# Performance work log

Hardware: AMD Instinct MI355X
Metric: run time of the kernel (lower is better)

## Reference

```python
import jax, jax.numpy as jnp
import numpy as np

# Lorentz (hyperboloid) manifold, curvature parameter K: x0 = sqrt(K + ||x_space||^2)
K = 1.0
LN_EPS = 1e-5
PROJ_EPS = 1e-6
L, D, H, B, S, V = 12, 512, 8, 2, 1024, 50257
DH = D // H  # 64 space dims per head


def add_time(space):
    # lift space components onto the hyperboloid
    t = jnp.sqrt(jnp.sum(space * space, axis=-1, keepdims=True) + K)
    return jnp.concatenate([t, space], axis=-1)


def l_project(z):
    # renormalize an ambient vector onto the hyperboloid (Lorentz midpoint / LResNet normalization)
    inner = -jnp.square(z[..., :1]) + jnp.sum(jnp.square(z[..., 1:]), axis=-1, keepdims=True)
    return jnp.sqrt(K) * z / jnp.sqrt(jnp.clip(-inner, PROJ_EPS, None))


def l_layernorm(x, g, b):
    # LayerNorm on the space part, recompute time
    s = x[..., 1:]
    mu = jnp.mean(s, axis=-1, keepdims=True)
    var = jnp.var(s, axis=-1, keepdims=True)
    s = (s - mu) * jax.lax.rsqrt(var + LN_EPS) * g + b
    return add_time(s)


def setup_inputs() -> dict:
    key = jax.random.key(0)
    ks = jax.random.split(key, 12)
    std_in = D ** -0.5
    std_out = (2 * D * L) ** -0.5  # out_proj_std from the torch init
    inp = {}
    inp['text_tokens'] = jax.random.randint(ks[0], (B, S), 0, V)
    inp['embed_table'] = jax.random.normal(ks[1], (V, D - 1), jnp.float32) * 0.02
    inp['Wq'] = jax.random.normal(ks[2], (L, D, D), jnp.float32) * std_in
    inp['bq'] = jnp.zeros((L, D), jnp.float32)
    inp['Wk'] = jax.random.normal(ks[3], (L, D, D), jnp.float32) * std_in
    inp['bk'] = jnp.zeros((L, D), jnp.float32)
    inp['Wv'] = jax.random.normal(ks[4], (L, D, D), jnp.float32) * std_in
    inp['bv'] = jnp.zeros((L, D), jnp.float32)
    inp['Wo'] = jax.random.normal(ks[5], (L, H * (DH + 1), D - 1), jnp.float32) * std_in
    inp['bo'] = jnp.zeros((L, D - 1), jnp.float32)
    inp['ln1_g'] = jnp.ones((L, D - 1), jnp.float32)
    inp['ln1_b'] = jnp.zeros((L, D - 1), jnp.float32)
    inp['ln2_g'] = jnp.ones((L, D - 1), jnp.float32)
    inp['ln2_b'] = jnp.zeros((L, D - 1), jnp.float32)
    inp['Wfc'] = jax.random.normal(ks[6], (L, D, 4 * D - 1), jnp.float32) * std_in
    inp['bfc'] = jnp.zeros((L, 4 * D - 1), jnp.float32)
    inp['Wpr'] = jax.random.normal(ks[7], (L, 4 * D, D - 1), jnp.float32) * std_out
    inp['bpr'] = jnp.zeros((L, D - 1), jnp.float32)
    inp['res_w1'] = jnp.ones((L,), jnp.float32)
    inp['res_w2'] = jnp.ones((L,), jnp.float32)
    inp['Wfin'] = jax.random.normal(ks[8], (D, D - 1), jnp.float32) * std_in
    inp['bfin'] = jnp.zeros((D - 1,), jnp.float32)
    inp['lnf_g'] = jnp.ones((D - 1,), jnp.float32)
    inp['lnf_b'] = jnp.zeros((D - 1,), jnp.float32)
    return inp


def reference(text_tokens, embed_table, Wq, bq, Wk, bk, Wv, bv, Wo, bo, ln1_g, ln1_b,
              ln2_g, ln2_b, Wfc, bfc, Wpr, bpr, res_w1, res_w2, Wfin, bfin, lnf_g, lnf_b):
    b, s = text_tokens.shape
    scale = 1.0 / np.sqrt(DH)
    # LorentzEmbeddings: space-part lookup, time recomputed
    x = add_time(embed_table[text_tokens])  # [B, S, D]
    causal = jnp.tril(jnp.ones((s, s), bool))  # True = attend
    for i in range(L):
        # --- Lorentz multi-head self-attention ---
        lx = l_layernorm(x, ln1_g[i], ln1_b[i])
        q = add_time((lx @ Wq[i] + bq[i]).reshape(b, s, H, DH))  # [B,S,H,DH+1]
        k = add_time((lx @ Wk[i] + bk[i]).reshape(b, s, H, DH))
        v = add_time((lx @ Wv[i] + bv[i]).reshape(b, s, H, DH))
        qm = jnp.concatenate([-q[..., :1], q[..., 1:]], axis=-1)  # apply Minkowski metric
        linner = jnp.einsum('bihd,bjhd->bhij', qm, k)  # Lorentz inner product <q_i, k_j>_L
        scores = (2.0 * K + 2.0 * linner) * scale     # = -d_L^2(q,k)/sqrt(dh)
        scores = jnp.where(causal[None, None], scores, -1e9)
        a = jax.nn.softmax(scores, axis=-1)
        agg = jnp.einsum('bhij,bjhd->bihd', a, v)      # Lorentz centroid numerator
        agg = l_project(agg)                           # normalize back to hyperboloid
        ax = add_time(agg.reshape(b, s, H * (DH + 1)) @ Wo[i] + bo[i])  # heads-concat proj
        x = l_project(x + res_w1[i] * ax)              # LResNet residual 1
        # --- Lorentz MLP ---
        h = l_layernorm(x, ln2_g[i], ln2_b[i])
        h = add_time(h @ Wfc[i] + bfc[i])              # c_fc: D -> 4D ambient
        h = add_time(jax.nn.gelu(h[..., 1:]))          # LorentzActivation (GELU on space)
        h = add_time(h @ Wpr[i] + bpr[i])              # c_proj: 4D -> D ambient
        x = l_project(x + res_w2[i] * h)               # LResNet residual 2
    x = add_time(x @ Wfin + bfin)                      # final_proj
    x = l_layernorm(x, lnf_g, lnf_b)                   # ln_final
    return x
```

## Files before the change

kernel.cpp:

```cpp
#include <hip/hip_runtime.h>
#include <cstdint>

#define DEV __device__ __forceinline__

typedef _Float16 f16;
typedef _Float16 f16x8 __attribute__((ext_vector_type(8)));
typedef float f32x4 __attribute__((ext_vector_type(4)));
typedef unsigned int u32;

DEV void gll16(const void* g, void* l) {
  __builtin_amdgcn_global_load_lds((const __attribute__((address_space(1))) u32*)g,
                                   (__attribute__((address_space(3))) u32*)l, 16, 0, 0);
}

DEV float block_sum(float v, float* red) {
#pragma unroll
  for (int o = 32; o; o >>= 1) v += __shfl_xor(v, o);
  int w = threadIdx.x >> 6;
  __syncthreads();
  if ((threadIdx.x & 63) == 0) red[w] = v;
  __syncthreads();
  return red[0] + red[1] + red[2] + red[3];
}

__global__ void k_trans(const float* __restrict__ W0, f16* __restrict__ BT0, int K, int N, int Kpad,
                        size_t srcStride, size_t dstStride) {
  __shared__ float t[32][33];
  const float* W = W0 + (size_t)blockIdx.z * srcStride;
  f16* BT = BT0 + (size_t)blockIdx.z * dstStride;
  int n0 = blockIdx.x * 32, k0 = blockIdx.y * 32, tx = threadIdx.x, ty = threadIdx.y;
  for (int i = ty; i < 32; i += 8) {
    int k = k0 + i, n = n0 + tx;
    t[i][tx] = (k < K && n < N) ? W[(size_t)k * N + n] : 0.f;
  }
  __syncthreads();
  for (int i = ty; i < 32; i += 8)
    BT[(size_t)(n0 + i) * Kpad + k0 + tx] = (f16)t[tx][i];
}

__global__ void k_trans3(const float* __restrict__ Wq, const float* __restrict__ Wk,
                         const float* __restrict__ Wv, f16* __restrict__ BT) {
  __shared__ float t[32][33];
  const int layer = blockIdx.z / 3, typ = blockIdx.z % 3;
  const float* W = ((typ == 0) ? Wq : (typ == 1) ? Wk : Wv) + (size_t)layer * 262144;
  f16* dst = BT + (size_t)layer * 786432 + (size_t)typ * 262144;
  int n0 = blockIdx.x * 32, k0 = blockIdx.y * 32, tx = threadIdx.x, ty = threadIdx.y;
  for (int i = ty; i < 32; i += 8) t[i][tx] = W[(size_t)(k0 + i) * 512 + n0 + tx];
  __syncthreads();
  for (int i = ty; i < 32; i += 8) dst[(size_t)(n0 + i) * 512 + k0 + tx] = (f16)t[tx][i];
}

template <int BM, int BN, int EPI>
__launch_bounds__(256)
__global__ void k_gemm(const f16* __restrict__ A, const f16* __restrict__ BT,
                       int lda, int ldb, int klen,
                       float* __restrict__ O1, float* __restrict__ O2, int ldc,
                       const float* __restrict__ c0, const float* __restrict__ c1,
                       const float* __restrict__ c2, float* __restrict__ ssq,
                       f16* __restrict__ H1, f16* __restrict__ H2, f16* __restrict__ H3) {
  constexpr int FM = BM / 32, FN = BN / 32;
  __shared__ f16 sA[BM * 64];
  __shared__ f16 sB[BN * 64];
  const int tid = threadIdx.x, wid = tid >> 6, lane = tid & 63;
  const int l15 = lane & 15, l4 = lane >> 4;
  const int m0 = blockIdx.x * BM, n0 = blockIdx.y * BN;
  const int wm = wid >> 1, wn = wid & 1;
  const int kbeg = blockIdx.z * klen;
  f32x4 acc[FM][FN];
#pragma unroll
  for (int i = 0; i < FM; i++)
#pragma unroll
    for (int j = 0; j < FN; j++) acc[i][j] = (f32x4){0.f, 0.f, 0.f, 0.f};
  const size_t ldab = (size_t)lda * 2, ldbb = (size_t)ldb * 2;
  const int swz = ((lane & 7) ^ (lane >> 3)) * 16;
  const char* Ab = (const char*)A + (size_t)m0 * ldab + (size_t)(lane >> 3) * ldab + swz;
  const char* Bb = (const char*)BT + (size_t)n0 * ldbb + (size_t)(lane >> 3) * ldbb + swz;
  for (int k0 = kbeg; k0 < kbeg + klen; k0 += 64) {
    for (int i = wid; i < BM / 8; i += 4)
      gll16(Ab + (size_t)(i * 8) * ldab + (size_t)k0 * 2, (char*)sA + i * 1024);
    for (int i = wid; i < BN / 8; i += 4)
      gll16(Bb + (size_t)(i * 8) * ldbb + (size_t)k0 * 2, (char*)sB + i * 1024);
    __syncthreads();
#pragma unroll
    for (int kk = 0; kk < 2; kk++) {
      f16x8 af[FM], bf[FN];
#pragma unroll
      for (int i = 0; i < FM; i++) {
        int row = wm * (BM / 2) + i * 16 + l15;
        af[i] = *(const f16x8*)(sA + row * 64 + (((kk * 4 + l4) ^ (l15 & 7)) * 8));
      }
#pragma unroll
      for (int j = 0; j < FN; j++) {
        int row = wn * (BN / 2) + j * 16 + l15;
        bf[j] = *(const f16x8*)(sB + row * 64 + (((kk * 4 + l4) ^ (l15 & 7)) * 8));
      }
#pragma unroll
      for (int i = 0; i < FM; i++)
#pragma unroll
        for (int j = 0; j < FN; j++)
          acc[i][j] = __builtin_amdgcn_mfma_f32_16x16x32_f16(af[i], bf[j], acc[i][j], 0, 0, 0);
    }
    __syncthreads();
  }
  if (EPI == 0) {
#pragma unroll
    for (int i = 0; i < FM; i++) {
      int row0 = m0 + wm * (BM / 2) + i * 16 + l4 * 4;
#pragma unroll
      for (int j = 0; j < FN; j++) {
        int col = n0 + wn * (BN / 2) + j * 16 + l15;
#pragma unroll
        for (int r = 0; r < 4; r++) O1[(size_t)(row0 + r) * ldc + col] = acc[i][j][r];
      }
    }
  } else if (EPI == 1) {
    const int cb = (n0 >> 6) + wn;
    const int typ = cb >> 3, h = cb & 7;
    const float* bb = (typ == 0) ? c0 : (typ == 1) ? c1 : c2;
    float bias_j[FN];
#pragma unroll
    for (int j = 0; j < FN; j++) bias_j[j] = bb[h * 64 + j * 16 + l15];
    const float qs = (typ == 0) ? 0.25f : 1.0f;
#pragma unroll
    for (int i = 0; i < FM; i++) {
#pragma unroll
      for (int r = 0; r < 4; r++) {
        float y[FN];
        float ss = 0.f;
#pragma unroll
        for (int j = 0; j < FN; j++) {
          y[j] = acc[i][j][r] + bias_j[j];
          ss += y[j] * y[j];
        }
        ss += __shfl_xor(ss, 1); ss += __shfl_xor(ss, 2);
        ss += __shfl_xor(ss, 4); ss += __shfl_xor(ss, 8);
        float t = sqrtf(ss + 1.f);
        int row = m0 + wm * 64 + i * 16 + l4 * 4 + r;
        int b = row >> 10, s = row & 1023, bh = b * 8 + h;
        if (typ < 2) {
          f16* dst = (typ == 0) ? H1 : H2;
          size_t base = ((size_t)bh * 1024 + s) * 88;
#pragma unroll
          for (int j = 0; j < FN; j++) dst[base + j * 16 + l15] = (f16)(qs * y[j]);
          if (l15 == 0) dst[base + 64] = (f16)(qs * t);
        } else {
#pragma unroll
          for (int j = 0; j < FN; j++)
            H3[((size_t)bh * 80 + j * 16 + l15) * 1024 + s] = (f16)y[j];
          if (l15 == 0) H3[((size_t)bh * 80 + 64) * 1024 + s] = (f16)t;
        }
      }
    }
  } else if (EPI == 2) {
#pragma unroll
    for (int i = 0; i < FM; i++) {
#pragma unroll
      for (int r = 0; r < 4; r++) {
        int row = m0 + wm * 64 + i * 16 + l4 * 4 + r;
        float ss = 0.f;
#pragma unroll
        for (int j = 0; j < FN; j++) {
          int col = n0 + wn * 64 + j * 16 + l15;
          float gg = 0.f;
          if (col < 2047) {
            float yv = acc[i][j][r] + c0[col];
            float cc = yv * yv * yv;
            gg = 0.5f * yv * (1.f + tanhf(0.7978845608f * (yv + 0.044715f * cc)));
          }
          ss += gg * gg;
          H1[(size_t)row * 2048 + col] = (f16)gg;
        }
        ss += __shfl_xor(ss, 1); ss += __shfl_xor(ss, 2);
        ss += __shfl_xor(ss, 4); ss += __shfl_xor(ss, 8);
        if (l15 == 0) atomicAdd(ssq + row, ss);
      }
    }
  } else {
    float* O = blockIdx.z ? O2 : O1;
#pragma unroll
    for (int i = 0; i < FM; i++) {
#pragma unroll
      for (int r = 0; r < 4; r++) {
        int row = m0 + wm * (BM / 2) + i * 16 + l4 * 4 + r;
        float t = 0.f;
        if (blockIdx.z == 0) t = sqrtf(ssq[row] + 1.f);
#pragma unroll
        for (int j = 0; j < FN; j++) {
          int col = n0 + wn * (BN / 2) + j * 16 + l15;
          float v = acc[i][j][r];
          if (blockIdx.z == 0) v += t * ((col < 511) ? c0[col] : 0.f);
          O[(size_t)row * ldc + col] = v;
        }
      }
    }
  }
}

__global__ void k_embed(const int* __restrict__ tok, const float* __restrict__ tbl,
                        const float* __restrict__ g, const float* __restrict__ bsh,
                        float* __restrict__ x, f16* __restrict__ act) {
  __shared__ float red[4];
  const int m = blockIdx.x, tid = threadIdx.x;
  const float* e = tbl + (size_t)tok[m] * 511;
  float e0 = (tid < 511) ? e[tid] : 0.f;
  float e1 = (tid + 256 < 511) ? e[tid + 256] : 0.f;
  float s1 = block_sum(e0 + e1, red);
  float s2 = block_sum(e0 * e0 + e1 * e1, red);
  float t = sqrtf(s2 + 1.f);
  float* xr = x + (size_t)m * 512;
  if (tid == 0) xr[0] = t;
  if (tid < 511) xr[1 + tid] = e0;
  if (tid + 256 < 511) xr[257 + tid] = e1;
  float mu = s1 / 511.f;
  float var = s2 / 511.f - mu * mu;
  float inv = rsqrtf(var + 1e-5f);
  float n0 = (tid < 511) ? (e0 - mu) * inv * g[tid] + bsh[tid] : 0.f;
  float n1 = (tid + 256 < 511) ? (e1 - mu) * inv * g[tid + 256] + bsh[tid + 256] : 0.f;
  float sn = block_sum(n0 * n0 + n1 * n1, red);
  float t2 = sqrtf(sn + 1.f);
  f16* ar = act + (size_t)m * 512;
  if (tid == 0) ar[0] = (f16)t2;
  if (tid < 511) ar[1 + tid] = (f16)n0;
  if (tid + 256 < 511) ar[257 + tid] = (f16)n1;
}

__launch_bounds__(64)
__global__ void k_attn(const f16* __restrict__ qhat, const f16* __restrict__ khat,
                       const f16* __restrict__ vT, f16* __restrict__ ao) {
  __shared__ f16 sP[16 * 88];
  const int bid = blockIdx.x, bh = bid & 15, rt = 63 - (bid >> 4);
  const int lane = threadIdx.x, l15 = lane & 15, l4 = lane >> 4;
  const f16* qp = qhat + ((size_t)bh * 1024 + rt * 16) * 88;
  const f16* kp = khat + (size_t)bh * 1024 * 88;
  const f16* vp = vT + (size_t)bh * 80 * 1024;
  f16x8 qf0 = *(const f16x8*)(qp + l15 * 88 + l4 * 8);
  f16x8 qf1 = *(const f16x8*)(qp + l15 * 88 + 32 + l4 * 8);
  float qth[4];
#pragma unroll
  for (int r = 0; r < 4; r++) qth[r] = (float)qp[(l4 * 4 + r) * 88 + 64];
  f32x4 acc[5];
#pragma unroll
  for (int i = 0; i < 5; i++) acc[i] = (f32x4){0, 0, 0, 0};
  float mrun[4] = {-3e38f, -3e38f, -3e38f, -3e38f}, lrun[4] = {0, 0, 0, 0};
  const int nt = (rt >> 2) + 1;
  for (int jt = 0; jt < nt; ++jt) {
    const int j0 = jt * 64;
    const bool dt = (jt == nt - 1);
    f32x4 sc[4];
#pragma unroll
    for (int fn = 0; fn < 4; fn++) {
      const f16* kb = kp + (size_t)(j0 + fn * 16 + l15) * 88;
      f16x8 k0v = *(const f16x8*)(kb + l4 * 8);
      f16x8 k1v = *(const f16x8*)(kb + 32 + l4 * 8);
      f32x4 a = (f32x4){0, 0, 0, 0};
      a = __builtin_amdgcn_mfma_f32_16x16x32_f16(qf0, k0v, a, 0, 0, 0);
      a = __builtin_amdgcn_mfma_f32_16x16x32_f16(qf1, k1v, a, 0, 0, 0);
      sc[fn] = a;
    }
    float s[4][4];
#pragma unroll
    for (int fn = 0; fn < 4; fn++) {
      float ktc = (float)kp[(size_t)(j0 + fn * 16 + l15) * 88 + 64];
      int col = j0 + fn * 16 + l15;
#pragma unroll
      for (int r = 0; r < 4; r++) {
        int row = rt * 16 + l4 * 4 + r;
        float v = sc[fn][r] - qth[r] * ktc;
        s[fn][r] = (!dt || col <= row) ? v : -3e38f;
      }
    }
    float mnew[4], al[4], rs[4];
#pragma unroll
    for (int r = 0; r < 4; r++) {
      float t = fmaxf(fmaxf(s[0][r], s[1][r]), fmaxf(s[2][r], s[3][r]));
#pragma unroll
      for (int o = 8; o; o >>= 1) t = fmaxf(t, __shfl_xor(t, o));
      mnew[r] = fmaxf(mrun[r], t);
      al[r] = exp2f((mrun[r] - mnew[r]) * 1.44269504f);
      mrun[r] = mnew[r];
      rs[r] = 0.f;
    }
#pragma unroll
    for (int fn = 0; fn < 4; fn++)
#pragma unroll
      for (int r = 0; r < 4; r++) {
        float p = exp2f((s[fn][r] - mnew[r]) * 1.44269504f);
        rs[r] += p;
        sP[(l4 * 4 + r) * 88 + fn * 16 + l15] = (f16)p;
      }
#pragma unroll
    for (int r = 0; r < 4; r++) {
#pragma unroll
      for (int o = 8; o; o >>= 1) rs[r] += __shfl_xor(rs[r], o);
      lrun[r] = lrun[r] * al[r] + rs[r];
    }
#pragma unroll
    for (int fd = 0; fd < 5; fd++)
#pragma unroll
      for (int r = 0; r < 4; r++) acc[fd][r] *= al[r];
    __syncthreads();
#pragma unroll
    for (int ks = 0; ks < 2; ks++) {
      f16x8 pf = *(const f16x8*)(sP + l15 * 88 + ks * 32 + l4 * 8);
#pragma unroll
      for (int fd = 0; fd < 5; fd++) {
        f16x8 vf = *(const f16x8*)(vp + (size_t)(fd * 16 + l15) * 1024 + j0 + ks * 32 + l4 * 8);
        acc[fd] = __builtin_amdgcn_mfma_f32_16x16x32_f16(pf, vf, acc[fd], 0, 0, 0);
      }
    }
    __syncthreads();
  }
  const int b = bh >> 3, h = bh & 7;
#pragma unroll
  for (int r = 0; r < 4; r++) {
    float invl = 1.0f / lrun[r];
    float ss = 0.f;
    float ov[4];
#pragma unroll
    for (int fd = 0; fd < 4; fd++) {
      ov[fd] = acc[fd][r] * invl;
      ss += ov[fd] * ov[fd];
    }
#pragma unroll
    for (int o = 8; o; o >>= 1) ss += __shfl_xor(ss, o);
    float tv = acc[4][r] * invl;
    tv = __shfl(tv, lane & 48);
    float scp = rsqrtf(fmaxf(tv * tv - ss, 1e-6f));
    int row = rt * 16 + l4 * 4 + r;
    size_t rowbase = ((size_t)b * 1024 + row) * 576;
    size_t rb = rowbase + h * 65;
    if (l15 == 0) ao[rb] = (f16)(tv * scp);
#pragma unroll
    for (int fd = 0; fd < 4; fd++) ao[rb + 1 + fd * 16 + l15] = (f16)(ov[fd] * scp);
    for (int c = l15; c < 56; c += 16) ao[rowbase + 520 + c] = (f16)0.f;
  }
}

__global__ void k_resproj(float* __restrict__ x, const float* __restrict__ r1,
                          const float* __restrict__ r2, int useR2,
                          const float* __restrict__ bias, const float* __restrict__ resw, int li,
                          const float* __restrict__ g, const float* __restrict__ bsh,
                          f16* __restrict__ act, int applyLN, float* __restrict__ ssq) {
  __shared__ float red[4];
  const int m = blockIdx.x, tid = threadIdx.x;
  const float* ra = r1 + (size_t)m * 512;
  const float* rb = r2 + (size_t)m * 512;
  float* xr = x + (size_t)m * 512;
  const float rw = resw[li];
  if (tid == 0) ssq[m] = 0.f;
  float y0 = 0.f, y1 = 0.f;
  if (tid < 511) { y0 = ra[tid] + bias[tid]; if (useR2) y0 += rb[tid]; }
  if (tid + 256 < 511) { y1 = ra[tid + 256] + bias[tid + 256]; if (useR2) y1 += rb[tid + 256]; }
  float s2 = block_sum(y0 * y0 + y1 * y1, red);
  float tax = sqrtf(s2 + 1.f);
  float xt = xr[0];
  float u0 = (tid < 511) ? xr[1 + tid] + rw * y0 : 0.f;
  float u1 = (tid + 256 < 511) ? xr[257 + tid] + rw * y1 : 0.f;
  float ut = xt + rw * tax;
  float su = block_sum(u0 + u1, red);
  float su2 = block_sum(u0 * u0 + u1 * u1, red);
  float scp = rsqrtf(fmaxf(ut * ut - su2, 1e-6f));
  float nx0 = u0 * scp, nx1 = u1 * scp, nxt = ut * scp;
  if (tid == 0) xr[0] = nxt;
  if (tid < 511) xr[1 + tid] = nx0;
  if (tid + 256 < 511) xr[257 + tid] = nx1;
  f16* ar = act + (size_t)m * 512;
  if (applyLN) {
    float mu = su * scp / 511.f;
    float var = su2 * scp * scp / 511.f - mu * mu;
    float inv = rsqrtf(var + 1e-5f);
    float n0 = (tid < 511) ? (nx0 - mu) * inv * g[tid] + bsh[tid] : 0.f;
    float n1 = (tid + 256 < 511) ? (nx1 - mu) * inv * g[tid + 256] + bsh[tid + 256] : 0.f;
    float sn = block_sum(n0 * n0 + n1 * n1, red);
    float t2 = sqrtf(sn + 1.f);
    if (tid == 0) ar[0] = (f16)t2;
    if (tid < 511) ar[1 + tid] = (f16)n0;
    if (tid + 256 < 511) ar[257 + tid] = (f16)n1;
  } else {
    if (tid == 0) ar[0] = (f16)nxt;
    if (tid < 511) ar[1 + tid] = (f16)nx0;
    if (tid + 256 < 511) ar[257 + tid] = (f16)nx1;
  }
}

__global__ void k_final(const float* __restrict__ raw, const float* __restrict__ bias,
                        const float* __restrict__ g, const float* __restrict__ bsh,
                        float* __restrict__ out) {
  __shared__ float red[4];
  const int m = blockIdx.x, tid = threadIdx.x;
  const float* rr = raw + (size_t)m * 512;
  float y0 = (tid < 511) ? rr[tid] + bias[tid] : 0.f;
  float y1 = (tid + 256 < 511) ? rr[tid + 256] + bias[tid + 256] : 0.f;
  float s1 = block_sum(y0 + y1, red);
  float s2 = block_sum(y0 * y0 + y1 * y1, red);
  float mu = s1 / 511.f;
  float var = s2 / 511.f - mu * mu;
  float inv = rsqrtf(var + 1e-5f);
  float n0 = (tid < 511) ? (y0 - mu) * inv * g[tid] + bsh[tid] : 0.f;
  float n1 = (tid + 256 < 511) ? (y1 - mu) * inv * g[tid + 256] + bsh[tid + 256] : 0.f;
  float sn = block_sum(n0 * n0 + n1 * n1, red);
  float t2 = sqrtf(sn + 1.f);
  float* orow = out + (size_t)m * 512;
  if (tid == 0) orow[0] = t2;
  if (tid < 511) orow[1 + tid] = n0;
  if (tid + 256 < 511) orow[257 + tid] = n1;
}

extern "C" void kernel_launch(void* const* d_in, const int* in_sizes, int n_in,
                              void* d_out, int out_size, void* d_ws, size_t ws_size,
                              hipStream_t stream) {
  (void)in_sizes; (void)n_in; (void)out_size; (void)ws_size;
  const int* tok = (const int*)d_in[0];
  const float* etab = (const float*)d_in[1];
  const float* Wq = (const float*)d_in[2];
  const float* bq = (const float*)d_in[3];
  const float* Wk = (const float*)d_in[4];
  const float* bk = (const float*)d_in[5];
  const float* Wv = (const float*)d_in[6];
  const float* bv = (const float*)d_in[7];
  const float* Wo = (const float*)d_in[8];
  const float* bo = (const float*)d_in[9];
  const float* ln1g = (const float*)d_in[10];
  const float* ln1b = (const float*)d_in[11];
  const float* ln2g = (const float*)d_in[12];
  const float* ln2b = (const float*)d_in[13];
  const float* Wfc = (const float*)d_in[14];
  const float* bfc = (const float*)d_in[15];
  const float* Wpr = (const float*)d_in[16];
  const float* bpr = (const float*)d_in[17];
  const float* rw1 = (const float*)d_in[18];
  const float* rw2 = (const float*)d_in[19];
  const float* Wfin = (const float*)d_in[20];
  const float* bfin = (const float*)d_in[21];
  const float* lnfg = (const float*)d_in[22];
  const float* lnfb = (const float*)d_in[23];

  char* wsb = (char*)d_ws;
  size_t off = 0;
  auto alloc = [&](size_t bytes) -> char* {
    char* p = wsb + off;
    off = (off + bytes + 1023) & ~(size_t)1023;
    return p;
  };
  float* x = (float*)alloc(2048ull * 512 * 4);
  f16* actA = (f16*)alloc(2048ull * 512 * 2);
  float* raw1 = (float*)alloc(2048ull * 512 * 4);
  float* raw2 = (float*)alloc(2048ull * 512 * 4);
  float* ssq = (float*)alloc(2048ull * 4);
  f16* qhat = (f16*)alloc(16ull * 1024 * 88 * 2);
  f16* khat = (f16*)alloc(16ull * 1024 * 88 * 2);
  f16* vT = (f16*)alloc(16ull * 80 * 1024 * 2);
  f16* ao = (f16*)alloc(2048ull * 576 * 2);
  f16* fcact = (f16*)alloc(2048ull * 2048 * 2);
  f16* wqkvT = (f16*)alloc(12ull * 1536 * 512 * 2);
  f16* woT = (f16*)alloc(12ull * 512 * 576 * 2);
  f16* wfcT = (f16*)alloc(12ull * 2048 * 512 * 2);
  f16* wprT = (f16*)alloc(12ull * 512 * 2048 * 2);
  f16* wfinT = (f16*)alloc(512ull * 512 * 2);

  k_trans3<<<dim3(16, 16, 36), dim3(32, 8), 0, stream>>>(Wq, Wk, Wv, wqkvT);
  k_trans<<<dim3(16, 18, 12), dim3(32, 8), 0, stream>>>(Wo, woT, 520, 511, 576,
                                                        520ull * 511, 512ull * 576);
  k_trans<<<dim3(64, 16, 12), dim3(32, 8), 0, stream>>>(Wfc, wfcT, 512, 2047, 512,
                                                        512ull * 2047, 2048ull * 512);
  k_trans<<<dim3(16, 64, 12), dim3(32, 8), 0, stream>>>(Wpr + 511, wprT, 2047, 511, 2048,
                                                        2048ull * 511, 512ull * 2048);
  k_trans<<<dim3(16, 16, 1), dim3(32, 8), 0, stream>>>(Wfin, wfinT, 512, 511, 512, 0, 0);

  k_embed<<<2048, 256, 0, stream>>>(tok, etab, ln1g, ln1b, x, actA);

  for (int li = 0; li < 12; li++) {
    const f16* wqkvT_l = wqkvT + (size_t)li * 1536 * 512;
    const f16* woT_l = woT + (size_t)li * 512 * 576;
    const f16* wfcT_l = wfcT + (size_t)li * 2048 * 512;
    const f16* wprT_l = wprT + (size_t)li * 512 * 2048;
    const float* Wpr_l = Wpr + (size_t)li * 2048 * 511;
    const float* bq_l = bq + (size_t)li * 512;
    const float* bk_l = bk + (size_t)li * 512;
    const float* bv_l = bv + (size_t)li * 512;
    const float* bo_l = bo + (size_t)li * 511;
    const float* bfc_l = bfc + (size_t)li * 2047;
    const float* bpr_l = bpr + (size_t)li * 511;
    const float* ln2g_l = ln2g + (size_t)li * 511;
    const float* ln2b_l = ln2b + (size_t)li * 511;

    k_gemm<128, 128, 1><<<dim3(16, 12, 1), 256, 0, stream>>>(
        actA, wqkvT_l, 512, 512, 512, nullptr, nullptr, 0,
        bq_l, bk_l, bv_l, nullptr, qhat, khat, vT);
    k_attn<<<1024, 64, 0, stream>>>(qhat, khat, vT, ao);
    k_gemm<64, 64, 0><<<dim3(32, 8, 1), 256, 0, stream>>>(
        ao, woT_l, 576, 576, 576, raw1, nullptr, 512,
        nullptr, nullptr, nullptr, nullptr, nullptr, nullptr, nullptr);
    k_resproj<<<2048, 256, 0, stream>>>(x, raw1, raw1, 0, bo_l, rw1, li,
                                        ln2g_l, ln2b_l, actA, 1, ssq);
    k_gemm<128, 128, 2><<<dim3(16, 16, 1), 256, 0, stream>>>(
        actA, wfcT_l, 512, 512, 512, nullptr, nullptr, 0,
        bfc_l, nullptr, nullptr, ssq, fcact, nullptr, nullptr);
    k_gemm<64, 64, 3><<<dim3(32, 8, 2), 256, 0, stream>>>(
        fcact, wprT_l, 2048, 2048, 1024, raw1, raw2, 512,
        Wpr_l, nullptr, nullptr, ssq, nullptr, nullptr, nullptr);
    const float* ng = (li < 11) ? ln1g + (size_t)(li + 1) * 511 : ln1g;
    const float* nb = (li < 11) ? ln1b + (size_t)(li + 1) * 511 : ln1b;
    k_resproj<<<2048, 256, 0, stream>>>(x, raw1, raw2, 1, bpr_l, rw2, li,
                                        ng, nb, actA, (li < 11) ? 1 : 0, ssq);
  }

  k_gemm<64, 64, 0><<<dim3(32, 8, 1), 256, 0, stream>>>(
      actA, wfinT, 512, 512, 512, raw1, nullptr, 512,
      nullptr, nullptr, nullptr, nullptr, nullptr, nullptr, nullptr);
  k_final<<<2048, 256, 0, stream>>>(raw1, bfin, lnfg, lnfb, (float*)d_out);
}
```

Before: 1.650 ms.

## Double-buffer GEMM LDS loads, remap blocks across XCDs, split-K four for c_proj

The GEMM kernel now stages the next 64-wide K slice into a second LDS buffer while the current one is consumed, synchronising with explicit vmcnt waits and raw barriers instead of a load-then-sync loop. 128-row tiles run with 8 waves per block. Block indices are remapped so neighbouring tiles land on the same XCD, in both the GEMM and the attention kernel. The c_proj GEMM goes from split-K 2 to split-K 4, with four partial buffers summed in the residual kernel. Attention also drops its per-iteration block barriers, which is safe because the block is a single wave. The aim is to hide global-load latency and improve cache locality and occupancy, at the cost of more LDS per block and extra partial-sum traffic.

```diff
diff --git a/kernel.cpp b/kernel.cpp
--- a/kernel.cpp
+++ b/kernel.cpp
@@ -1,12 +1,12 @@
 #include <hip/hip_runtime.h>
 #include <cstdint>
-
-#define DEV __device__ __forceinline__
 
 typedef _Float16 f16;
 typedef _Float16 f16x8 __attribute__((ext_vector_type(8)));
 typedef float f32x4 __attribute__((ext_vector_type(4)));
 typedef unsigned int u32;
+
+#define DEV __device__ __forceinline__
 
 DEV void gll16(const void* g, void* l) {
   __builtin_amdgcn_global_load_lds((const __attribute__((address_space(1))) u32*)g,
@@ -50,65 +50,93 @@
   for (int i = ty; i < 32; i += 8) dst[(size_t)(n0 + i) * 512 + k0 + tx] = (f16)t[tx][i];
 }
 
-template <int BM, int BN, int EPI>
-__launch_bounds__(256)
-__global__ void k_gemm(const f16* __restrict__ A, const f16* __restrict__ BT,
-                       int lda, int ldb, int klen,
-                       float* __restrict__ O1, float* __restrict__ O2, int ldc,
-                       const float* __restrict__ c0, const float* __restrict__ c1,
-                       const float* __restrict__ c2, float* __restrict__ ssq,
-                       f16* __restrict__ H1, f16* __restrict__ H2, f16* __restrict__ H3) {
-  constexpr int FM = BM / 32, FN = BN / 32;
-  __shared__ f16 sA[BM * 64];
-  __shared__ f16 sB[BN * 64];
+template <int BM, int BN, int KZ, int EPI>
+__global__ __launch_bounds__((BM == 128) ? 512 : 256)
+void k_gemm(const f16* __restrict__ A, const f16* __restrict__ B,
+            int lda, int ldb, int klen, int GM,
+            float* __restrict__ O1, float* __restrict__ O2,
+            float* __restrict__ O3, float* __restrict__ O4, int ldc,
+            const float* __restrict__ c0, const float* __restrict__ c1,
+            const float* __restrict__ c2, float* __restrict__ ssq,
+            f16* __restrict__ H1, f16* __restrict__ H2, f16* __restrict__ H3) {
+  constexpr int NW = (BM == 128) ? 8 : 4;
+  constexpr int WM = (BM == 128) ? 4 : 2;
+  constexpr int FN = BN / ((NW / WM) * 16);
   const int tid = threadIdx.x, wid = tid >> 6, lane = tid & 63;
   const int l15 = lane & 15, l4 = lane >> 4;
-  const int m0 = blockIdx.x * BM, n0 = blockIdx.y * BN;
-  const int wm = wid >> 1, wn = wid & 1;
-  const int kbeg = blockIdx.z * klen;
-  f32x4 acc[FM][FN];
-#pragma unroll
-  for (int i = 0; i < FM; i++)
+  const int wm = wid % WM, wn = wid / WM;
+  const int nwg = gridDim.x;
+  int lin = blockIdx.x;
+  int wg = (lin & 7) * (nwg >> 3) + (lin >> 3);
+  int tn = wg / (GM * KZ);
+  int rem = wg - tn * (GM * KZ);
+  int tm = rem / KZ, tz = rem - (rem / KZ) * KZ;
+  const int m0 = tm * BM, n0 = tn * BN, kbeg = tz * klen, ksteps = klen / 64;
+  __shared__ __align__(16) char SM[(BM + BN) * 256];
+  f32x4 acc[2][FN];
+#pragma unroll
+  for (int i = 0; i < 2; i++)
 #pragma unroll
     for (int j = 0; j < FN; j++) acc[i][j] = (f32x4){0.f, 0.f, 0.f, 0.f};
   const size_t ldab = (size_t)lda * 2, ldbb = (size_t)ldb * 2;
   const int swz = ((lane & 7) ^ (lane >> 3)) * 16;
-  const char* Ab = (const char*)A + (size_t)m0 * ldab + (size_t)(lane >> 3) * ldab + swz;
-  const char* Bb = (const char*)BT + (size_t)n0 * ldbb + (size_t)(lane >> 3) * ldbb + swz;
-  for (int k0 = kbeg; k0 < kbeg + klen; k0 += 64) {
-    for (int i = wid; i < BM / 8; i += 4)
-      gll16(Ab + (size_t)(i * 8) * ldab + (size_t)k0 * 2, (char*)sA + i * 1024);
-    for (int i = wid; i < BN / 8; i += 4)
-      gll16(Bb + (size_t)(i * 8) * ldbb + (size_t)k0 * 2, (char*)sB + i * 1024);
-    __syncthreads();
+  const char* Ab = (const char*)A + (size_t)(m0 + (lane >> 3)) * ldab + swz + (size_t)kbeg * 2;
+  const char* Bb = (const char*)B + (size_t)(n0 + (lane >> 3)) * ldbb + swz + (size_t)kbeg * 2;
+  auto stage = [&](int buf, int ks) {
+    char* da = SM + buf * (BM * 128);
+    char* db = SM + 2 * BM * 128 + buf * (BN * 128);
+    for (int i = wid; i < BM / 8; i += NW)
+      gll16(Ab + (size_t)(i * 8) * ldab + (size_t)ks * 128, da + i * 1024);
+    for (int i = wid; i < BN / 8; i += NW)
+      gll16(Bb + (size_t)(i * 8) * ldbb + (size_t)ks * 128, db + i * 1024);
+  };
+  stage(0, 0);
+  asm volatile("s_waitcnt vmcnt(0)" ::: "memory");
+  __builtin_amdgcn_s_barrier();
+  __builtin_amdgcn_sched_barrier(0);
+  int cur = 0;
+  for (int ks = 0; ks < ksteps; ks++) {
+    const bool more = (ks + 1 < ksteps);
+    if (more) {
+      stage(cur ^ 1, ks + 1);
+      asm volatile("s_waitcnt vmcnt(4)" ::: "memory");
+    } else {
+      asm volatile("s_waitcnt vmcnt(0)" ::: "memory");
+    }
+    __builtin_amdgcn_s_barrier();
+    __builtin_amdgcn_sched_barrier(0);
+    const f16* sA = (const f16*)(SM + cur * (BM * 128));
+    const f16* sB = (const f16*)(SM + 2 * BM * 128 + cur * (BN * 128));
 #pragma unroll
     for (int kk = 0; kk < 2; kk++) {
-      f16x8 af[FM], bf[FN];
-#pragma unroll
-      for (int i = 0; i < FM; i++) {
-        int row = wm * (BM / 2) + i * 16 + l15;
+      f16x8 af[2], bf[FN];
+#pragma unroll
+      for (int i = 0; i < 2; i++) {
+        int row = wm * 32 + i * 16 + l15;
         af[i] = *(const f16x8*)(sA + row * 64 + (((kk * 4 + l4) ^ (l15 & 7)) * 8));
       }
 #pragma unroll
       for (int j = 0; j < FN; j++) {
-        int row = wn * (BN / 2) + j * 16 + l15;
+        int row = wn * (FN * 16) + j * 16 + l15;
         bf[j] = *(const f16x8*)(sB + row * 64 + (((kk * 4 + l4) ^ (l15 & 7)) * 8));
       }
 #pragma unroll
-      for (int i = 0; i < FM; i++)
+      for (int i = 0; i < 2; i++)
 #pragma unroll
         for (int j = 0; j < FN; j++)
           acc[i][j] = __builtin_amdgcn_mfma_f32_16x16x32_f16(af[i], bf[j], acc[i][j], 0, 0, 0);
     }
-    __syncthreads();
+    __builtin_amdgcn_sched_barrier(0);
+    __builtin_amdgcn_s_barrier();
+    cur ^= 1;
   }
   if (EPI == 0) {
 #pragma unroll
-    for (int i = 0; i < FM; i++) {
-      int row0 = m0 + wm * (BM / 2) + i * 16 + l4 * 4;
+    for (int i = 0; i < 2; i++) {
+      int row0 = m0 + wm * 32 + i * 16 + l4 * 4;
 #pragma unroll
       for (int j = 0; j < FN; j++) {
-        int col = n0 + wn * (BN / 2) + j * 16 + l15;
+        int col = n0 + wn * (FN * 16) + j * 16 + l15;
 #pragma unroll
         for (int r = 0; r < 4; r++) O1[(size_t)(row0 + r) * ldc + col] = acc[i][j][r];
       }
@@ -117,28 +145,24 @@
     const int cb = (n0 >> 6) + wn;
     const int typ = cb >> 3, h = cb & 7;
     const float* bb = (typ == 0) ? c0 : (typ == 1) ? c1 : c2;
-    float bias_j[FN];
-#pragma unroll
-    for (int j = 0; j < FN; j++) bias_j[j] = bb[h * 64 + j * 16 + l15];
+    float bj[FN];
+#pragma unroll
+    for (int j = 0; j < FN; j++) bj[j] = bb[h * 64 + j * 16 + l15];
     const float qs = (typ == 0) ? 0.25f : 1.0f;
 #pragma unroll
-    for (int i = 0; i < FM; i++) {
+    for (int i = 0; i < 2; i++) {
 #pragma unroll
       for (int r = 0; r < 4; r++) {
-        float y[FN];
-        float ss = 0.f;
-#pragma unroll
-        for (int j = 0; j < FN; j++) {
-          y[j] = acc[i][j][r] + bias_j[j];
-          ss += y[j] * y[j];
-        }
+        float y[FN], ss = 0.f;
+#pragma unroll
+        for (int j = 0; j < FN; j++) { y[j] = acc[i][j][r] + bj[j]; ss += y[j] * y[j]; }
         ss += __shfl_xor(ss, 1); ss += __shfl_xor(ss, 2);
         ss += __shfl_xor(ss, 4); ss += __shfl_xor(ss, 8);
         float t = sqrtf(ss + 1.f);
-        int row = m0 + wm * 64 + i * 16 + l4 * 4 + r;
+        int row = m0 + wm * 32 + i * 16 + l4 * 4 + r;
         int b = row >> 10, s = row & 1023, bh = b * 8 + h;
         if (typ < 2) {
-          f16* dst = (typ == 0) ? H1 : H2;
+          f16* dst = typ ? H2 : H1;
           size_t base = ((size_t)bh * 1024 + s) * 88;
 #pragma unroll
           for (int j = 0; j < FN; j++) dst[base + j * 16 + l15] = (f16)(qs * y[j]);
@@ -153,14 +177,14 @@
     }
   } else if (EPI == 2) {
 #pragma unroll
-    for (int i = 0; i < FM; i++) {
+    for (int i = 0; i < 2; i++) {
 #pragma unroll
       for (int r = 0; r < 4; r++) {
-        int row = m0 + wm * 64 + i * 16 + l4 * 4 + r;
+        int row = m0 + wm * 32 + i * 16 + l4 * 4 + r;
         float ss = 0.f;
 #pragma unroll
         for (int j = 0; j < FN; j++) {
-          int col = n0 + wn * 64 + j * 16 + l15;
+          int col = n0 + wn * (FN * 16) + j * 16 + l15;
           float gg = 0.f;
           if (col < 2047) {
             float yv = acc[i][j][r] + c0[col];
@@ -176,19 +200,19 @@
       }
     }
   } else {
-    float* O = blockIdx.z ? O2 : O1;
-#pragma unroll
-    for (int i = 0; i < FM; i++) {
+    float* O = (tz == 0) ? O1 : (tz == 1) ? O2 : (tz == 2) ? O3 : O4;
+#pragma unroll
+    for (int i = 0; i < 2; i++) {
 #pragma unroll
       for (int r = 0; r < 4; r++) {
-        int row = m0 + wm * (BM / 2) + i * 16 + l4 * 4 + r;
+        int row = m0 + wm * 32 + i * 16 + l4 * 4 + r;
         float t = 0.f;
-        if (blockIdx.z == 0) t = sqrtf(ssq[row] + 1.f);
+        if (tz == 0) t = sqrtf(ssq[row] + 1.f);
 #pragma unroll
         for (int j = 0; j < FN; j++) {
-          int col = n0 + wn * (BN / 2) + j * 16 + l15;
+          int col = n0 + wn * (FN * 16) + j * 16 + l15;
           float v = acc[i][j][r];
-          if (blockIdx.z == 0) v += t * ((col < 511) ? c0[col] : 0.f);
+          if (tz == 0) v += t * ((col < 511) ? c0[col] : 0.f);
           O[(size_t)row * ldc + col] = v;
         }
       }
@@ -228,7 +252,9 @@
 __global__ void k_attn(const f16* __restrict__ qhat, const f16* __restrict__ khat,
                        const f16* __restrict__ vT, f16* __restrict__ ao) {
   __shared__ f16 sP[16 * 88];
-  const int bid = blockIdx.x, bh = bid & 15, rt = 63 - (bid >> 4);
+  const int lin = blockIdx.x;
+  const int wg = (lin & 7) * 128 + (lin >> 3);
+  const int bh = wg >> 6, rt = 63 - (wg & 63);
   const int lane = threadIdx.x, l15 = lane & 15, l4 = lane >> 4;
   const f16* qp = qhat + ((size_t)bh * 1024 + rt * 16) * 88;
   const f16* kp = khat + (size_t)bh * 1024 * 88;
@@ -298,7 +324,8 @@
     for (int fd = 0; fd < 5; fd++)
 #pragma unroll
       for (int r = 0; r < 4; r++) acc[fd][r] *= al[r];
-    __syncthreads();
+    asm volatile("s_waitcnt lgkmcnt(0)" ::: "memory");
+    __builtin_amdgcn_sched_barrier(0);
 #pragma unroll
     for (int ks = 0; ks < 2; ks++) {
       f16x8 pf = *(const f16x8*)(sP + l15 * 88 + ks * 32 + l4 * 8);
@@ -308,19 +335,14 @@
         acc[fd] = __builtin_amdgcn_mfma_f32_16x16x32_f16(pf, vf, acc[fd], 0, 0, 0);
       }
     }
-    __syncthreads();
   }
   const int b = bh >> 3, h = bh & 7;
 #pragma unroll
   for (int r = 0; r < 4; r++) {
     float invl = 1.0f / lrun[r];
-    float ss = 0.f;
-    float ov[4];
-#pragma unroll
-    for (int fd = 0; fd < 4; fd++) {
-      ov[fd] = acc[fd][r] * invl;
-      ss += ov[fd] * ov[fd];
-    }
+    float ss = 0.f, ov[4];
+#pragma unroll
+    for (int fd = 0; fd < 4; fd++) { ov[fd] = acc[fd][r] * invl; ss += ov[fd] * ov[fd]; }
 #pragma unroll
     for (int o = 8; o; o >>= 1) ss += __shfl_xor(ss, o);
     float tv = acc[4][r] * invl;
@@ -337,20 +359,28 @@
 }
 
 __global__ void k_resproj(float* __restrict__ x, const float* __restrict__ r1,
-                          const float* __restrict__ r2, int useR2,
+                          const float* __restrict__ r2, const float* __restrict__ r3,
+                          const float* __restrict__ r4, int np,
                           const float* __restrict__ bias, const float* __restrict__ resw, int li,
                           const float* __restrict__ g, const float* __restrict__ bsh,
                           f16* __restrict__ act, int applyLN, float* __restrict__ ssq) {
   __shared__ float red[4];
   const int m = blockIdx.x, tid = threadIdx.x;
-  const float* ra = r1 + (size_t)m * 512;
-  const float* rb = r2 + (size_t)m * 512;
-  float* xr = x + (size_t)m * 512;
+  const size_t rb = (size_t)m * 512;
+  float* xr = x + rb;
   const float rw = resw[li];
   if (tid == 0) ssq[m] = 0.f;
   float y0 = 0.f, y1 = 0.f;
-  if (tid < 511) { y0 = ra[tid] + bias[tid]; if (useR2) y0 += rb[tid]; }
-  if (tid + 256 < 511) { y1 = ra[tid + 256] + bias[tid + 256]; if (useR2) y1 += rb[tid + 256]; }
+  if (tid < 511) {
+    y0 = r1[rb + tid];
+    if (np == 4) y0 += r2[rb + tid] + r3[rb + tid] + r4[rb + tid];
+    y0 += bias[tid];
+  }
+  if (tid + 256 < 511) {
+    y1 = r1[rb + tid + 256];
+    if (np == 4) y1 += r2[rb + tid + 256] + r3[rb + tid + 256] + r4[rb + tid + 256];
+    y1 += bias[tid + 256];
+  }
   float s2 = block_sum(y0 * y0 + y1 * y1, red);
   float tax = sqrtf(s2 + 1.f);
   float xt = xr[0];
@@ -364,7 +394,7 @@
   if (tid == 0) xr[0] = nxt;
   if (tid < 511) xr[1 + tid] = nx0;
   if (tid + 256 < 511) xr[257 + tid] = nx1;
-  f16* ar = act + (size_t)m * 512;
+  f16* ar = act + rb;
   if (applyLN) {
     float mu = su * scp / 511.f;
     float var = su2 * scp * scp / 511.f - mu * mu;
@@ -446,6 +476,8 @@
   f16* actA = (f16*)alloc(2048ull * 512 * 2);
   float* raw1 = (float*)alloc(2048ull * 512 * 4);
   float* raw2 = (float*)alloc(2048ull * 512 * 4);
+  float* raw3 = (float*)alloc(2048ull * 512 * 4);
+  float* raw4 = (float*)alloc(2048ull * 512 * 4);
   float* ssq = (float*)alloc(2048ull * 4);
   f16* qhat = (f16*)alloc(16ull * 1024 * 88 * 2);
   f16* khat = (f16*)alloc(16ull * 1024 * 88 * 2);
@@ -484,29 +516,29 @@
     const float* ln2g_l = ln2g + (size_t)li * 511;
     const float* ln2b_l = ln2b + (size_t)li * 511;
 
-    k_gemm<128, 128, 1><<<dim3(16, 12, 1), 256, 0, stream>>>(
-        actA, wqkvT_l, 512, 512, 512, nullptr, nullptr, 0,
+    k_gemm<128, 128, 1, 1><<<192, 512, 0, stream>>>(
+        actA, wqkvT_l, 512, 512, 512, 16, nullptr, nullptr, nullptr, nullptr, 0,
         bq_l, bk_l, bv_l, nullptr, qhat, khat, vT);
     k_attn<<<1024, 64, 0, stream>>>(qhat, khat, vT, ao);
-    k_gemm<64, 64, 0><<<dim3(32, 8, 1), 256, 0, stream>>>(
-        ao, woT_l, 576, 576, 576, raw1, nullptr, 512,
+    k_gemm<64, 64, 1, 0><<<256, 256, 0, stream>>>(
+        ao, woT_l, 576, 576, 576, 32, raw1, nullptr, nullptr, nullptr, 512,
         nullptr, nullptr, nullptr, nullptr, nullptr, nullptr, nullptr);
-    k_resproj<<<2048, 256, 0, stream>>>(x, raw1, raw1, 0, bo_l, rw1, li,
+    k_resproj<<<2048, 256, 0, stream>>>(x, raw1, raw1, raw1, raw1, 1, bo_l, rw1, li,
                                         ln2g_l, ln2b_l, actA, 1, ssq);
-    k_gemm<128, 128, 2><<<dim3(16, 16, 1), 256, 0, stream>>>(
-        actA, wfcT_l, 512, 512, 512, nullptr, nullptr, 0,
+    k_gemm<128, 128, 1, 2><<<256, 512, 0, stream>>>(
+        actA, wfcT_l, 512, 512, 512, 16, nullptr, nullptr, nullptr, nullptr, 0,
         bfc_l, nullptr, nullptr, ssq, fcact, nullptr, nullptr);
-    k_gemm<64, 64, 3><<<dim3(32, 8, 2), 256, 0, stream>>>(
-        fcact, wprT_l, 2048, 2048, 1024, raw1, raw2, 512,
+    k_gemm<64, 64, 4, 3><<<1024, 256, 0, stream>>>(
+        fcact, wprT_l, 2048, 2048, 512, 32, raw1, raw2, raw3, raw4, 512,
         Wpr_l, nullptr, nullptr, ssq, nullptr, nullptr, nullptr);
     const float* ng = (li < 11) ? ln1g + (size_t)(li + 1) * 511 : ln1g;
     const float* nb = (li < 11) ? ln1b + (size_t)(li + 1) * 511 : ln1b;
-    k_resproj<<<2048, 256, 0, stream>>>(x, raw1, raw2, 1, bpr_l, rw2, li,
+    k_resproj<<<2048, 256, 0, stream>>>(x, raw1, raw2, raw3, raw4, 4, bpr_l, rw2, li,
                                         ng, nb, actA, (li < 11) ? 1 : 0, ssq);
   }
 
-  k_gemm<64, 64, 0><<<dim3(32, 8, 1), 256, 0, stream>>>(
-      actA, wfinT, 512, 512, 512, raw1, nullptr, 512,
+  k_gemm<64, 64, 1, 0><<<256, 256, 0, stream>>>(
+      actA, wfinT, 512, 512, 512, 32, raw1, nullptr, nullptr, nullptr, 512,
       nullptr, nullptr, nullptr, nullptr, nullptr, nullptr, nullptr);
   k_final<<<2048, 256, 0, stream>>>(raw1, bfin, lnfg, lnfb, (float*)d_out);
 }
```

New measurement: 1.630 ms. About the same (-1.2%).
